# Kernel tuning notes

Measured on AMD Instinct MI355X. Metric: run time of the kernel, lower is better.

Reference implementation:

```python
import jax, jax.numpy as jnp
import numpy as np

B, N, D = 64, 1024, 512
H, LD = 8, 64            # num_heads, linear_hidden_dim (H*LD == D)
HIDDEN = 4 * D           # ffn_multiply = 4.0
NB = 128                 # number of timestamp buckets
EPS = 1e-6
TS_SCALE = NB / 14.0     # log1p(1e6) ~ 13.8 -> buckets span [0, NB]


def rms_norm(x, eps=EPS):
    return x * jax.lax.rsqrt(jnp.mean(x * x, axis=-1, keepdims=True) + eps)


def setup_inputs() -> dict:
    key = jax.random.key(0)
    ks = jax.random.split(key, 8)
    lengths = np.linspace(256, N, B).astype(np.int64)
    x_offsets = jnp.asarray(np.concatenate([[0], np.cumsum(lengths)]), dtype=jnp.int64)
    T = int(lengths.sum())
    x = jax.random.normal(ks[0], (T, D), dtype=jnp.float32)
    all_timestamps = jnp.sort(jax.random.randint(ks[1], (B, N), 0, 10**6, dtype=jnp.int64), axis=1)
    invalid_attn_mask = jnp.tril(jnp.ones((N, N), jnp.float32))  # causal
    uv = jax.random.normal(ks[2], (D, 3 * H * LD), dtype=jnp.float32) * 0.02
    pos_w = jax.random.normal(ks[3], (2 * N - 1,), dtype=jnp.float32) * 0.02
    ts_w = jax.random.normal(ks[4], (NB + 1,), dtype=jnp.float32) * 0.02
    w_ams = jax.random.normal(ks[5], (2 * H * LD, D), dtype=jnp.float32) * 0.02
    w1 = jax.random.normal(ks[6], (D, HIDDEN), dtype=jnp.float32) * 0.02
    w2 = jax.random.normal(ks[7], (HIDDEN, D), dtype=jnp.float32) * 0.02
    return {"x": x, "x_offsets": x_offsets, "all_timestamps": all_timestamps,
            "invalid_attn_mask": invalid_attn_mask, "uv": uv, "pos_w": pos_w,
            "ts_w": ts_w, "w_ams": w_ams, "w1": w1, "w2": w2}


def reference(x, x_offsets, all_timestamps, invalid_attn_mask, uv, pos_w, ts_w, w_ams, w1, w2):
    T = x.shape[0]
    # RMSNorm (no learned scale, matches F.rms_norm with no weight) + fused proj + SiLU
    proj = jax.nn.silu(rms_norm(x) @ uv)                       # [T, 3*H*LD]
    u, v = proj[:, :2 * H * LD], proj[:, 2 * H * LD:]          # [T,2HD'], [T,HD']
    # jagged -> padded dense
    tok = jnp.arange(T)
    seg = jnp.searchsorted(x_offsets, tok, side="right") - 1   # batch id per token
    pos = tok - x_offsets[seg]                                  # position within sequence
    padded_v = jnp.zeros((B, N, H * LD), v.dtype).at[seg, pos].set(v).reshape(B, N, H, LD)
    # positional relative bias (batch-independent)
    rel = jnp.arange(N)[:, None] - jnp.arange(N)[None, :]
    pos_attn = pos_w[rel + N - 1] * invalid_attn_mask           # [N,N]
    # temporal relative bias: log-bucketized |t_i - t_j|
    dt = jnp.abs(all_timestamps[:, :, None] - all_timestamps[:, None, :]).astype(jnp.float32)
    bucket = jnp.clip(jnp.floor(jnp.log1p(dt) * TS_SCALE), 0, NB).astype(jnp.int32)
    ts_attn = ts_w[bucket] * invalid_attn_mask[None]            # [B,N,N]
    # two-stream bias 'attention' (no softmax)
    out_pos = jnp.einsum("nm,bmhd->bnhd", pos_attn, padded_v)
    out_ts = jnp.einsum("bnm,bmhd->bnhd", ts_attn, padded_v)
    combined = jnp.concatenate([out_pos, out_ts], axis=-1).reshape(B, N, 2 * H * LD)
    attn_out = combined[seg, pos]                               # dense -> jagged, [T, 2*H*LD]
    # gated norm + multistage FFN with residuals
    ams = u * rms_norm(attn_out)
    h = x + ams @ w_ams
    out = h + jax.nn.silu(rms_norm(h) @ w1) @ w2
    return out
```

## Files before the change

### kernel.cpp

```cpp
#include <hip/hip_runtime.h>
#include <cmath>


using u16 = unsigned short;
using u8  = unsigned char;

typedef __bf16 bf16x8 __attribute__((ext_vector_type(8)));
typedef float  f32x4  __attribute__((ext_vector_type(4)));

#define TS_SCALE_F (float)(128.0 / 14.0)

__device__ __forceinline__ u16 f2b(float f) {
  unsigned u = __float_as_uint(f);
  unsigned r = 0x7FFFu + ((u >> 16) & 1u);
  return (u16)((u + r) >> 16);
}
__device__ __forceinline__ float b2f(u16 v) {
  return __uint_as_float(((unsigned)v) << 16);
}
__device__ __forceinline__ bf16x8 as_frag(uint4 r) {
  union { uint4 u; bf16x8 v; } c; c.u = r; return c.v;
}

__device__ __forceinline__ void gload_lds16(const u16* g, u16* l) {
  __builtin_amdgcn_global_load_lds(
      (const __attribute__((address_space(1))) unsigned int*)g,
      (__attribute__((address_space(3))) unsigned int*)l, 16, 0, 0);
}

__device__ __forceinline__ size_t ts_base_u8(int b, int nt) {
  return (size_t)b * 589824 + (size_t)(nt * (nt + 1) / 2) * 16384;
}

__global__ __launch_bounds__(256) void wprep(
    const float* __restrict__ W, u16* __restrict__ Wp, int K, int N)
{
  const int p = blockIdx.x, s = blockIdx.y;
  const int t = threadIdx.x;
  size_t base = ((size_t)p * (K >> 5) + s) * 4096;
  const int e0 = t * 16;
  u16 o[16];
#pragma unroll
  for (int i = 0; i < 16; ++i) {
    int e = e0 + i;
    int kb = e >> 10, r = e & 1023, c = r >> 3, ke = r & 7;
    o[i] = f2b(W[(size_t)(s * 32 + kb * 8 + ke) * N + p * 128 + c]);
  }
  *(uint4*)(Wp + base + e0)     = *(uint4*)o;
  *(uint4*)(Wp + base + e0 + 8) = *(uint4*)(o + 8);
}

#define EPI_SILU_BF16 0
#define EPI_ADD_F32   1
#define AM_BF16   0
#define AM_F32S   1
#define AM_BF16SM 2

template <int EPI, int AMODE>
__global__ __launch_bounds__(256, 2) void gemm_bf16(
    const u16* __restrict__ A, const float* __restrict__ Af,
    const float* __restrict__ inv, const u16* __restrict__ U, int ustride,
    const u16* __restrict__ Wp, void* __restrict__ C,
    const float* __restrict__ ADD, int M, int N, int K, int ncb)
{
  __shared__ u16 lA[128 * 40];
  __shared__ u16 lB[4096];

  const int nblk = gridDim.x;
  const int q = nblk >> 3, r = nblk & 7;
  const int xcd = blockIdx.x & 7, li = blockIdx.x >> 3;
  const int work = xcd * q + (xcd < r ? xcd : r) + li;
  const int c0b = work % ncb;
  const int t0  = (work / ncb) * 128;
  const int c0  = c0b * 128;

  const int tid  = threadIdx.x;
  const int wave = tid >> 6, lane = tid & 63;
  const int wr   = (wave >> 1) * 64, wc = (wave & 1) * 64;
  const int l15  = lane & 15, l4 = lane >> 4;

  f32x4 z = {0.f, 0.f, 0.f, 0.f};
  f32x4 acc[4][4];
#pragma unroll
  for (int m = 0; m < 4; ++m)
#pragma unroll
    for (int j = 0; j < 4; ++j) acc[m][j] = z;

  const int ar = tid >> 1, ak = (tid & 1) * 16;
  const int row = t0 + ar;
  const bool arow_ok = row < M;
  float rinv = 0.f;
  if (AMODE != AM_BF16 && arow_ok) rinv = inv[row];
  const u16*   ab = (AMODE != AM_F32S) ? A + (size_t)row * K + ak : nullptr;
  const float* af = (AMODE == AM_F32S) ? Af + (size_t)row * K + ak : nullptr;
  const u16*   um = (AMODE == AM_BF16SM) ? U + (size_t)row * ustride + ak : nullptr;

  const int ksteps = K >> 5;
  const u16* wsrc = Wp + (size_t)c0b * ksteps * 4096 + wave * 1024 + lane * 8;
  u16* ldsb = &lB[wave * 1024];

  for (int s = 0; s < ksteps; ++s) {
    const int k0 = s * 32;
    uint4 pr[4];
    const uint4 z4 = make_uint4(0, 0, 0, 0);
    if (!arow_ok) { pr[0] = z4; pr[1] = z4; pr[2] = z4; pr[3] = z4; }
    else if constexpr (AMODE == AM_BF16) {
      pr[0] = *(const uint4*)(ab + k0);
      pr[1] = *(const uint4*)(ab + k0 + 8);
    } else if constexpr (AMODE == AM_F32S) {
      pr[0] = *(const uint4*)(af + k0);
      pr[1] = *(const uint4*)(af + k0 + 4);
      pr[2] = *(const uint4*)(af + k0 + 8);
      pr[3] = *(const uint4*)(af + k0 + 12);
    } else {
      pr[0] = *(const uint4*)(ab + k0);
      pr[1] = *(const uint4*)(ab + k0 + 8);
      pr[2] = *(const uint4*)(um + k0);
      pr[3] = *(const uint4*)(um + k0 + 8);
    }
    gload_lds16(wsrc,       ldsb);
    gload_lds16(wsrc + 512, ldsb + 512);
    wsrc += 4096;
    {
      u16 tmp[16];
      if constexpr (AMODE == AM_BF16) {
        *(uint4*)tmp       = pr[0];
        *(uint4*)(tmp + 8) = pr[1];
      } else if constexpr (AMODE == AM_F32S) {
        const float* f = (const float*)pr;
#pragma unroll
        for (int i = 0; i < 16; ++i) tmp[i] = f2b(f[i] * rinv);
      } else {
        const u16* a = (const u16*)pr;
        const u16* u = (const u16*)(pr + 2);
#pragma unroll
        for (int i = 0; i < 16; ++i) tmp[i] = f2b(b2f(a[i]) * rinv * b2f(u[i]));
      }
      *(uint4*)&lA[ar * 40 + ak]     = *(uint4*)tmp;
      *(uint4*)&lA[ar * 40 + ak + 8] = *(uint4*)(tmp + 8);
    }
    __syncthreads();

    bf16x8 afr[4], bfv[4];
#pragma unroll
    for (int m = 0; m < 4; ++m)
      afr[m] = as_frag(*(const uint4*)&lA[(wr + m * 16 + l15) * 40 + l4 * 8]);
#pragma unroll
    for (int j = 0; j < 4; ++j)
      bfv[j] = as_frag(*(const uint4*)&lB[(l4 << 10) + (wc + j * 16 + l15) * 8]);
#pragma unroll
    for (int m = 0; m < 4; ++m)
#pragma unroll
      for (int j = 0; j < 4; ++j)
        acc[m][j] = __builtin_amdgcn_mfma_f32_16x16x32_bf16(afr[m], bfv[j], acc[m][j], 0, 0, 0);
    __syncthreads();
  }

#pragma unroll
  for (int m = 0; m < 4; ++m) {
#pragma unroll
    for (int rr = 0; rr < 4; ++rr) {
      int orow = t0 + wr + m * 16 + l4 * 4 + rr;
      if (orow >= M) continue;
#pragma unroll
      for (int j = 0; j < 4; ++j) {
        int col = c0 + wc + j * 16 + l15;
        size_t idx = (size_t)orow * N + col;
        float y = acc[m][j][rr];
        if constexpr (EPI == EPI_SILU_BF16) {
          float s = y / (1.f + __expf(-y));
          ((u16*)C)[idx] = f2b(s);
        } else {
          ((float*)C)[idx] = y + ADD[idx];
        }
      }
    }
  }
}

__global__ __launch_bounds__(128) void pos_scores(
    const float* __restrict__ pos_w, u16* __restrict__ pos_s)
{
  const int n = blockIdx.x;
  const int m0 = threadIdx.x * 8;
  u16 o[8];
#pragma unroll
  for (int i = 0; i < 8; ++i) {
    int m = m0 + i;
    float v = (m <= n) ? pos_w[n - m + 1023] : 0.f;
    o[i] = f2b(v);
  }
  *(uint4*)(pos_s + (size_t)n * 1024 + m0) = *(uint4*)o;
}

__global__ __launch_bounds__(256) void ts_buckets(
    const int* __restrict__ tstamp, u8* __restrict__ ts_s)
{
  const int nt = 7 - (blockIdx.x >> 6);
  const int b  = blockIdx.x & 63;
  const int W  = 128 * (nt + 1);
  const int n0 = nt * 128;
  const int tid = threadIdx.x;

  __shared__ int tsm[1024];
  for (int i = tid; i < W; i += 256) tsm[i] = tstamp[b * 1024 + i];
  __syncthreads();

  const int r = tid >> 1, h = tid & 1;
  const int n_abs = n0 + r;
  const int t_n = tstamp[b * 1024 + n_abs];
  const int half = W >> 1;
  const int c0 = h * half;
  u8* row = ts_s + ts_base_u8(b, nt) + (size_t)r * W + c0;

  for (int c = 0; c < half; c += 16) {
    u8 o[16];
#pragma unroll
    for (int i = 0; i < 16; ++i) {
      int m = c0 + c + i;
      int d = t_n - tsm[m];
      if (d < 0) d = -d;
      int bkt = (int)(log1pf((float)d) * TS_SCALE_F);
      bkt = bkt > 128 ? 128 : bkt;
      o[i] = (m <= n_abs) ? (u8)bkt : (u8)129;
    }
    *(uint4*)(row + c) = *(uint4*)o;
  }
}

__global__ __launch_bounds__(256, 1) void attn_gemm(
    const u16* __restrict__ proj,
    const int* __restrict__ xoff,
    const u16* __restrict__ pos_s,
    const u8*  __restrict__ tsU8,
    const float* __restrict__ ts_w,
    u16* __restrict__ attn_out,
    int Ttot)
{
  const int flat = blockIdx.x;
  const int nt = 7 - (flat >> 8);
  const int rem = flat & 255;
  const int b  = rem >> 2;
  const int ct = rem & 3;

  const int off = xoff[b];
  int len = xoff[b + 1] - off;
  if (len < 0) len = 0;
  if (len > 1024) len = 1024;
  if (off < 0 || off + len > Ttot) return;
  const int n0 = nt * 128;
  if (n0 >= len) return;
  const int c0 = ct * 128;
  const int W = 128 * (nt + 1);

  __shared__ u16 lP[128 * 40];
  __shared__ u16 lT[128 * 40];
  __shared__ u16 sV[4096];
  __shared__ float s_tsw[130];

  const int tid = threadIdx.x;
  if (tid < 130) s_tsw[tid] = (tid < 129) ? ts_w[tid] : 0.f;
  __syncthreads();

  const int wave = tid >> 6, lane = tid & 63;
  const int wr = (wave >> 1) * 64, wc = (wave & 1) * 64;
  const int l15 = lane & 15, l4 = lane >> 4;

  f32x4 z = {0.f, 0.f, 0.f, 0.f};
  f32x4 accP[4][4], accT[4][4];
#pragma unroll
  for (int m = 0; m < 4; ++m)
#pragma unroll
    for (int j = 0; j < 4; ++j) { accP[m][j] = z; accT[m][j] = z; }

  const int ar = tid >> 1, ak = (tid & 1) * 16;
  const u16* pRow = pos_s + (size_t)(n0 + ar) * 1024 + ak;
  const u8*  tRow = tsU8 + ts_base_u8(b, nt) + (size_t)ar * W + ak;
  const int vk = tid >> 3, vc = (tid & 7) * 16;

  const int mEnd = (n0 + 128 < len) ? (n0 + 128) : len;

  for (int m0 = 0; m0 < mEnd; m0 += 32) {
    {
      int mm = m0 + vk;
      uint4 v0 = make_uint4(0, 0, 0, 0), v1 = v0;
      if (mm < len) {
        const u16* src = proj + (size_t)(off + mm) * 1536 + 1024 + c0 + vc;
        v0 = *(const uint4*)src;
        v1 = *(const uint4*)(src + 8);
      }
      u16 tmp[16];
      *(uint4*)tmp       = v0;
      *(uint4*)(tmp + 8) = v1;
      const int kb = vk >> 3, ke = vk & 7;
#pragma unroll
      for (int i = 0; i < 16; ++i) {
        int col = vc + i;
        int o2 = (kb * 2048 + col * 16 + ke * 2) ^ (((col >> 3) & 7) << 4);
        *(u16*)((char*)sV + o2) = tmp[i];
      }
    }
    {
      uint4 p0 = *(const uint4*)(pRow + m0);
      uint4 p1 = *(const uint4*)(pRow + m0 + 8);
      uint4 tb = *(const uint4*)(tRow + m0);
      u16 tt[16];
      const u8* bp = (const u8*)&tb;
#pragma unroll
      for (int i = 0; i < 16; ++i) tt[i] = f2b(s_tsw[bp[i]]);
      int wb = ar * 40 + ak;
      *(uint4*)&lP[wb]     = p0;
      *(uint4*)&lP[wb + 8] = p1;
      *(uint4*)&lT[wb]     = *(uint4*)tt;
      *(uint4*)&lT[wb + 8] = *(uint4*)(tt + 8);
    }
    __syncthreads();

    bf16x8 ap[4], at[4], bv[4];
#pragma unroll
    for (int m = 0; m < 4; ++m) {
      ap[m] = as_frag(*(const uint4*)&lP[(wr + m * 16 + l15) * 40 + l4 * 8]);
      at[m] = as_frag(*(const uint4*)&lT[(wr + m * 16 + l15) * 40 + l4 * 8]);
    }
#pragma unroll
    for (int j = 0; j < 4; ++j) {
      int col = wc + j * 16 + l15;
      int o2 = (l4 * 2048 + col * 16) ^ (((col >> 3) & 7) << 4);
      bv[j] = as_frag(*(const uint4*)((char*)sV + o2));
    }
#pragma unroll
    for (int m = 0; m < 4; ++m)
#pragma unroll
      for (int j = 0; j < 4; ++j) {
        accP[m][j] = __builtin_amdgcn_mfma_f32_16x16x32_bf16(ap[m], bv[j], accP[m][j], 0, 0, 0);
        accT[m][j] = __builtin_amdgcn_mfma_f32_16x16x32_bf16(at[m], bv[j], accT[m][j], 0, 0, 0);
      }
    __syncthreads();
  }

#pragma unroll
  for (int m = 0; m < 4; ++m)
#pragma unroll
    for (int r = 0; r < 4; ++r) {
      int n = n0 + wr + m * 16 + l4 * 4 + r;
      if (n >= len) continue;
      size_t t = (size_t)(off + n);
#pragma unroll
      for (int j = 0; j < 4; ++j) {
        int hd = c0 + wc + j * 16 + l15;
        int colP = ((hd >> 6) << 7) + (hd & 63);
        attn_out[t * 1024 + colP]      = f2b(accP[m][j][r]);
        attn_out[t * 1024 + colP + 64] = f2b(accT[m][j][r]);
      }
    }
}

template <int D, bool F32IN>
__global__ __launch_bounds__(256) void row_ss(
    const void* __restrict__ in, float* __restrict__ inv, int T)
{
  const int row = blockIdx.x * 4 + (threadIdx.x >> 6);
  const int lane = threadIdx.x & 63;
  if (row >= T) return;
  float ss = 0.f;
  if constexpr (F32IN) {
    const float* r = (const float*)in + (size_t)row * D;
#pragma unroll
    for (int i = lane * 4; i < D; i += 256) {
      float4 v = *(const float4*)(r + i);
      ss += v.x * v.x + v.y * v.y + v.z * v.z + v.w * v.w;
    }
  } else {
    const u16* r = (const u16*)in + (size_t)row * D;
#pragma unroll
    for (int i = lane * 8; i < D; i += 512) {
      uint4 v = *(const uint4*)(r + i);
      const u16* q = (const u16*)&v;
#pragma unroll
      for (int k = 0; k < 8; ++k) { float f = b2f(q[k]); ss += f * f; }
    }
  }
#pragma unroll
  for (int o = 32; o > 0; o >>= 1) ss += __shfl_down(ss, o, 64);
  if (lane == 0) inv[row] = rsqrtf(ss / (float)D + 1e-6f);
}

extern "C" void kernel_launch(void* const* d_in, const int* in_sizes, int n_in,
                              void* d_out, int out_size, void* d_ws, size_t ws_size,
                              hipStream_t stream)
{
  const float* x      = (const float*)d_in[0];
  const int*   xoff   = (const int*)d_in[1];
  const int*   tstamp = (const int*)d_in[2];
  const float* uv     = (const float*)d_in[4];
  const float* pos_w  = (const float*)d_in[5];
  const float* ts_w   = (const float*)d_in[6];
  const float* w_ams  = (const float*)d_in[7];
  const float* w1     = (const float*)d_in[8];
  const float* w2     = (const float*)d_in[9];
  const int T = in_sizes[0] / 512;
  const int nrow = (T + 127) / 128;

  char* ws = (char*)d_ws;
  size_t o = 0;
  auto take = [&](size_t bytes) { size_t r = o; o += (bytes + 255) & ~(size_t)255; return r; };

  u16* uvb    = (u16*)(ws + take((size_t)512 * 1536 * 2));
  u16* wamsb  = (u16*)(ws + take((size_t)1024 * 512 * 2));
  u16* w1b    = (u16*)(ws + take((size_t)512 * 2048 * 2));
  u16* w2b    = (u16*)(ws + take((size_t)2048 * 512 * 2));
  u16* posS   = (u16*)(ws + take((size_t)1024 * 1024 * 2));

  size_t o_ts   = take((size_t)64 * 589824);
  size_t o_attn = take((size_t)T * 1024 * 2);
  size_t o_proj = take((size_t)T * 1536 * 2);
  float* invX = (float*)(ws + take((size_t)T * 4));
  float* invA = (float*)(ws + take((size_t)T * 4));
  float* invH = (float*)(ws + take((size_t)T * 4));

  u8*  tsU8  = (u8*)(ws + o_ts);
  u16* attnS = (u16*)(ws + o_attn);
  u16* proj  = (u16*)(ws + o_proj);
  u16* mid   = (u16*)(ws + o_ts);
  float* h   = (float*)d_out;

  if (ws_size < o) return;

  wprep<<<dim3(12, 16), 256, 0, stream>>>(uv,    uvb,   512,  1536);
  wprep<<<dim3(4, 32),  256, 0, stream>>>(w_ams, wamsb, 1024, 512);
  wprep<<<dim3(16, 16), 256, 0, stream>>>(w1,    w1b,   512,  2048);
  wprep<<<dim3(4, 64),  256, 0, stream>>>(w2,    w2b,   2048, 512);

  pos_scores<<<1024, 128, 0, stream>>>(pos_w, posS);
  ts_buckets<<<512, 256, 0, stream>>>(tstamp, tsU8);

  row_ss<512, true><<<(T + 3) / 4, 256, 0, stream>>>(x, invX, T);

  gemm_bf16<EPI_SILU_BF16, AM_F32S><<<12 * nrow, 256, 0, stream>>>(
      nullptr, x, invX, nullptr, 0, uvb, proj, nullptr, T, 1536, 512, 12);

  attn_gemm<<<64 * 32, 256, 0, stream>>>(proj, xoff, posS, tsU8, ts_w, attnS, T);

  row_ss<1024, false><<<(T + 3) / 4, 256, 0, stream>>>(attnS, invA, T);

  gemm_bf16<EPI_ADD_F32, AM_BF16SM><<<4 * nrow, 256, 0, stream>>>(
      attnS, nullptr, invA, proj, 1536, wamsb, h, x, T, 512, 1024, 4);

  row_ss<512, true><<<(T + 3) / 4, 256, 0, stream>>>(h, invH, T);

  gemm_bf16<EPI_SILU_BF16, AM_F32S><<<16 * nrow, 256, 0, stream>>>(
      nullptr, h, invH, nullptr, 0, w1b, mid, nullptr, T, 2048, 512, 16);

  gemm_bf16<EPI_ADD_F32, AM_BF16><<<4 * nrow, 256, 0, stream>>>(
      mid, nullptr, nullptr, nullptr, 0, w2b, h, h, T, 512, 2048, 4);
}
```

Measured before the change: 855.2 us.

## Pre-pack V into MFMA layout and stream it via direct-to-LDS loads

Adds a vprep kernel that repacks the V slice of proj into the MFMA B-fragment tile layout, staged in the output buffer. attn_gemm can then fetch V with global_load_lds instead of scalar swizzled LDS stores. It also remaps block indices so consecutive blocks spread across XCDs, and switches bf16 rounding to the hardware packed convert. The costs are an extra kernel launch with a strided repack pass, and the output buffer now serves as scratch space.

New measurement: 877.8 us. 1.03x slower.

```diff
diff --git a/kernel.cpp b/kernel.cpp
--- a/kernel.cpp
+++ b/kernel.cpp
@@ -6,7 +6,9 @@
 using u8  = unsigned char;
 
 typedef __bf16 bf16x8 __attribute__((ext_vector_type(8)));
+typedef __bf16 bf16x2 __attribute__((ext_vector_type(2)));
 typedef float  f32x4  __attribute__((ext_vector_type(4)));
+typedef float  f32x2  __attribute__((ext_vector_type(2)));
 
 #define TS_SCALE_F (float)(128.0 / 14.0)
 
@@ -14,6 +16,14 @@
   unsigned u = __float_as_uint(f);
   unsigned r = 0x7FFFu + ((u >> 16) & 1u);
   return (u16)((u + r) >> 16);
+}
+__device__ __forceinline__ u16 f2b_n(float f) {
+  union { __bf16 b; u16 u; } c; c.b = (__bf16)f; return c.u;
+}
+__device__ __forceinline__ unsigned cvt_pk2(float a, float b) {
+  f32x2 v; v[0] = a; v[1] = b;
+  bf16x2 r = __builtin_convertvector(v, bf16x2);
+  union { bf16x2 b; unsigned u; } c; c.b = r; return c.u;
 }
 __device__ __forceinline__ float b2f(u16 v) {
   return __uint_as_float(((unsigned)v) << 16);
@@ -48,6 +58,38 @@
   }
   *(uint4*)(Wp + base + e0)     = *(uint4*)o;
   *(uint4*)(Wp + base + e0 + 8) = *(uint4*)(o + 8);
+}
+
+__global__ __launch_bounds__(256) void vprep(
+    const u16* __restrict__ proj, const int* __restrict__ xoff,
+    u16* __restrict__ Vp, int Ttot)
+{
+  const int b = blockIdx.x >> 5, rb = blockIdx.x & 31;
+  const int off = xoff[b];
+  int len = xoff[b + 1] - off;
+  if (len < 0) len = 0;
+  if (len > 1024) len = 1024;
+  if (off < 0 || off + len > Ttot) return;
+  if (rb * 32 >= len) return;
+  const int t = threadIdx.x;
+  size_t base = ((size_t)(b * 32 + rb)) * 4 * 4096;
+  const int e0 = t * 16;
+#pragma unroll
+  for (int ct = 0; ct < 4; ++ct) {
+    u16 o[16];
+#pragma unroll
+    for (int i = 0; i < 16; ++i) {
+      int e = e0 + i;
+      int kb = e >> 10, r = e & 1023, c = r >> 3, ke = r & 7;
+      int row = rb * 32 + kb * 8 + ke;
+      u16 v = 0;
+      if (row < len)
+        v = proj[(size_t)(off + row) * 1536 + 1024 + ct * 128 + c];
+      o[i] = v;
+    }
+    *(uint4*)(Vp + base + ct * 4096 + e0)     = *(uint4*)o;
+    *(uint4*)(Vp + base + ct * 4096 + e0 + 8) = *(uint4*)(o + 8);
+  }
 }
 
 #define EPI_SILU_BF16 0
@@ -123,18 +165,22 @@
     wsrc += 4096;
     {
       u16 tmp[16];
+      unsigned* t32 = (unsigned*)tmp;
       if constexpr (AMODE == AM_BF16) {
         *(uint4*)tmp       = pr[0];
         *(uint4*)(tmp + 8) = pr[1];
       } else if constexpr (AMODE == AM_F32S) {
         const float* f = (const float*)pr;
 #pragma unroll
-        for (int i = 0; i < 16; ++i) tmp[i] = f2b(f[i] * rinv);
+        for (int i = 0; i < 8; ++i)
+          t32[i] = cvt_pk2(f[2 * i] * rinv, f[2 * i + 1] * rinv);
       } else {
         const u16* a = (const u16*)pr;
         const u16* u = (const u16*)(pr + 2);
 #pragma unroll
-        for (int i = 0; i < 16; ++i) tmp[i] = f2b(b2f(a[i]) * rinv * b2f(u[i]));
+        for (int i = 0; i < 8; ++i)
+          t32[i] = cvt_pk2(b2f(a[2 * i]) * rinv * b2f(u[2 * i]),
+                           b2f(a[2 * i + 1]) * rinv * b2f(u[2 * i + 1]));
       }
       *(uint4*)&lA[ar * 40 + ak]     = *(uint4*)tmp;
       *(uint4*)&lA[ar * 40 + ak + 8] = *(uint4*)(tmp + 8);
@@ -169,7 +215,7 @@
         float y = acc[m][j][rr];
         if constexpr (EPI == EPI_SILU_BF16) {
           float s = y / (1.f + __expf(-y));
-          ((u16*)C)[idx] = f2b(s);
+          ((u16*)C)[idx] = f2b_n(s);
         } else {
           ((float*)C)[idx] = y + ADD[idx];
         }
@@ -229,7 +275,7 @@
 }
 
 __global__ __launch_bounds__(256, 1) void attn_gemm(
-    const u16* __restrict__ proj,
+    const u16* __restrict__ Vp,
     const int* __restrict__ xoff,
     const u16* __restrict__ pos_s,
     const u8*  __restrict__ tsU8,
@@ -237,11 +283,11 @@
     u16* __restrict__ attn_out,
     int Ttot)
 {
-  const int flat = blockIdx.x;
-  const int nt = 7 - (flat >> 8);
-  const int rem = flat & 255;
-  const int b  = rem >> 2;
-  const int ct = rem & 3;
+  const int li = blockIdx.x >> 3, xcd = blockIdx.x & 7;
+  const int sblk = xcd + (li >> 2) * 8;
+  const int ct = li & 3;
+  const int nt = 7 - (sblk >> 6);
+  const int b  = sblk & 63;
 
   const int off = xoff[b];
   int len = xoff[b + 1] - off;
@@ -276,43 +322,29 @@
   const int ar = tid >> 1, ak = (tid & 1) * 16;
   const u16* pRow = pos_s + (size_t)(n0 + ar) * 1024 + ak;
   const u8*  tRow = tsU8 + ts_base_u8(b, nt) + (size_t)ar * W + ak;
-  const int vk = tid >> 3, vc = (tid & 7) * 16;
+  const u16* vbase = Vp + ((size_t)(b * 32) * 4 + ct) * 4096 + wave * 1024 + lane * 8;
+  u16* ldsv = &sV[wave * 1024];
 
   const int mEnd = (n0 + 128 < len) ? (n0 + 128) : len;
 
   for (int m0 = 0; m0 < mEnd; m0 += 32) {
-    {
-      int mm = m0 + vk;
-      uint4 v0 = make_uint4(0, 0, 0, 0), v1 = v0;
-      if (mm < len) {
-        const u16* src = proj + (size_t)(off + mm) * 1536 + 1024 + c0 + vc;
-        v0 = *(const uint4*)src;
-        v1 = *(const uint4*)(src + 8);
-      }
-      u16 tmp[16];
-      *(uint4*)tmp       = v0;
-      *(uint4*)(tmp + 8) = v1;
-      const int kb = vk >> 3, ke = vk & 7;
-#pragma unroll
-      for (int i = 0; i < 16; ++i) {
-        int col = vc + i;
-        int o2 = (kb * 2048 + col * 16 + ke * 2) ^ (((col >> 3) & 7) << 4);
-        *(u16*)((char*)sV + o2) = tmp[i];
-      }
-    }
+    const u16* vsrc = vbase + (size_t)(m0 >> 5) * 16384;
+    gload_lds16(vsrc,       ldsv);
+    gload_lds16(vsrc + 512, ldsv + 512);
     {
       uint4 p0 = *(const uint4*)(pRow + m0);
       uint4 p1 = *(const uint4*)(pRow + m0 + 8);
       uint4 tb = *(const uint4*)(tRow + m0);
-      u16 tt[16];
       const u8* bp = (const u8*)&tb;
-#pragma unroll
-      for (int i = 0; i < 16; ++i) tt[i] = f2b(s_tsw[bp[i]]);
+      unsigned tt32[8];
+#pragma unroll
+      for (int i = 0; i < 8; ++i)
+        tt32[i] = cvt_pk2(s_tsw[bp[2 * i]], s_tsw[bp[2 * i + 1]]);
       int wb = ar * 40 + ak;
       *(uint4*)&lP[wb]     = p0;
       *(uint4*)&lP[wb + 8] = p1;
-      *(uint4*)&lT[wb]     = *(uint4*)tt;
-      *(uint4*)&lT[wb + 8] = *(uint4*)(tt + 8);
+      *(uint4*)&lT[wb]     = *(uint4*)tt32;
+      *(uint4*)&lT[wb + 8] = *(uint4*)(tt32 + 4);
     }
     __syncthreads();
 
@@ -323,11 +355,8 @@
       at[m] = as_frag(*(const uint4*)&lT[(wr + m * 16 + l15) * 40 + l4 * 8]);
     }
 #pragma unroll
-    for (int j = 0; j < 4; ++j) {
-      int col = wc + j * 16 + l15;
-      int o2 = (l4 * 2048 + col * 16) ^ (((col >> 3) & 7) << 4);
-      bv[j] = as_frag(*(const uint4*)((char*)sV + o2));
-    }
+    for (int j = 0; j < 4; ++j)
+      bv[j] = as_frag(*(const uint4*)&sV[(l4 << 10) + (wc + j * 16 + l15) * 8]);
 #pragma unroll
     for (int m = 0; m < 4; ++m)
 #pragma unroll
@@ -349,8 +378,8 @@
       for (int j = 0; j < 4; ++j) {
         int hd = c0 + wc + j * 16 + l15;
         int colP = ((hd >> 6) << 7) + (hd & 63);
-        attn_out[t * 1024 + colP]      = f2b(accP[m][j][r]);
-        attn_out[t * 1024 + colP + 64] = f2b(accT[m][j][r]);
+        attn_out[t * 1024 + colP]      = f2b_n(accP[m][j][r]);
+        attn_out[t * 1024 + colP + 64] = f2b_n(accT[m][j][r]);
       }
     }
 }
@@ -411,7 +440,7 @@
   u16* w2b    = (u16*)(ws + take((size_t)2048 * 512 * 2));
   u16* posS   = (u16*)(ws + take((size_t)1024 * 1024 * 2));
 
-  size_t o_ts   = take((size_t)64 * 589824);
+  size_t o_ts   = take((size_t)64 * 589824 + 256);
   size_t o_attn = take((size_t)T * 1024 * 2);
   size_t o_proj = take((size_t)T * 1536 * 2);
   float* invX = (float*)(ws + take((size_t)T * 4));
@@ -422,6 +451,7 @@
   u16* attnS = (u16*)(ws + o_attn);
   u16* proj  = (u16*)(ws + o_proj);
   u16* mid   = (u16*)(ws + o_ts);
+  u16*   Vp  = (u16*)d_out;
   float* h   = (float*)d_out;
 
   if (ws_size < o) return;
@@ -439,7 +469,9 @@
   gemm_bf16<EPI_SILU_BF16, AM_F32S><<<12 * nrow, 256, 0, stream>>>(
       nullptr, x, invX, nullptr, 0, uvb, proj, nullptr, T, 1536, 512, 12);
 
-  attn_gemm<<<64 * 32, 256, 0, stream>>>(proj, xoff, posS, tsU8, ts_w, attnS, T);
+  vprep<<<2048, 256, 0, stream>>>(proj, xoff, Vp, T);
+
+  attn_gemm<<<64 * 32, 256, 0, stream>>>(Vp, xoff, posS, tsU8, ts_w, attnS, T);
 
   row_ss<1024, false><<<(T + 3) / 4, 256, 0, stream>>>(attnS, invA, T);
 
```

## Double GEMM K-step to 64 and use native packed bf16 conversion

Applied to the files above, without the earlier changes.

Each GEMM main-loop iteration now stages a K-depth of 64 instead of 32, enlarging the A and B LDS tiles and running two MFMA sub-steps per barrier pair. This halves the number of __syncthreads and loop iterations per tile, at the cost of more LDS and registers per block, which may hurt occupancy at 2 blocks/CU. Manual round-to-nearest-even bf16 conversions are also replaced with compiler vector conversions (packed cvt) in the GEMM prologue, the epilogues and the attention T-matrix build. The workspace ts region gets 256 bytes of padding.

New measurement: 906.4 us. 6.0% more time.

```diff
diff --git a/kernel.cpp b/kernel.cpp
--- a/kernel.cpp
+++ b/kernel.cpp
@@ -6,7 +6,9 @@
 using u8  = unsigned char;
 
 typedef __bf16 bf16x8 __attribute__((ext_vector_type(8)));
+typedef __bf16 bf16x2 __attribute__((ext_vector_type(2)));
 typedef float  f32x4  __attribute__((ext_vector_type(4)));
+typedef float  f32x2  __attribute__((ext_vector_type(2)));
 
 #define TS_SCALE_F (float)(128.0 / 14.0)
 
@@ -14,6 +16,14 @@
   unsigned u = __float_as_uint(f);
   unsigned r = 0x7FFFu + ((u >> 16) & 1u);
   return (u16)((u + r) >> 16);
+}
+__device__ __forceinline__ u16 f2b_n(float f) {
+  union { __bf16 b; u16 u; } c; c.b = (__bf16)f; return c.u;
+}
+__device__ __forceinline__ unsigned cvt_pk2(float a, float b) {
+  f32x2 v; v[0] = a; v[1] = b;
+  bf16x2 r = __builtin_convertvector(v, bf16x2);
+  union { bf16x2 b; unsigned u; } c; c.b = r; return c.u;
 }
 __device__ __forceinline__ float b2f(u16 v) {
   return __uint_as_float(((unsigned)v) << 16);
@@ -63,8 +73,8 @@
     const u16* __restrict__ Wp, void* __restrict__ C,
     const float* __restrict__ ADD, int M, int N, int K, int ncb)
 {
-  __shared__ u16 lA[128 * 40];
-  __shared__ u16 lB[4096];
+  __shared__ u16 lA[128 * 72];
+  __shared__ u16 lB[8192];
 
   const int nblk = gridDim.x;
   const int q = nblk >> 3, r = nblk & 7;
@@ -86,7 +96,7 @@
 #pragma unroll
     for (int j = 0; j < 4; ++j) acc[m][j] = z;
 
-  const int ar = tid >> 1, ak = (tid & 1) * 16;
+  const int ar = tid >> 1, ak = (tid & 1) * 32;
   const int row = t0 + ar;
   const bool arow_ok = row < M;
   float rinv = 0.f;
@@ -95,64 +105,74 @@
   const float* af = (AMODE == AM_F32S) ? Af + (size_t)row * K + ak : nullptr;
   const u16*   um = (AMODE == AM_BF16SM) ? U + (size_t)row * ustride + ak : nullptr;
 
-  const int ksteps = K >> 5;
-  const u16* wsrc = Wp + (size_t)c0b * ksteps * 4096 + wave * 1024 + lane * 8;
-  u16* ldsb = &lB[wave * 1024];
-
-  for (int s = 0; s < ksteps; ++s) {
-    const int k0 = s * 32;
-    uint4 pr[4];
+  const int rounds = K >> 6;
+  const u16* wsrc = Wp + (size_t)c0b * (K >> 5) * 4096 + wave * 2048 + lane * 8;
+  u16* ldsb = &lB[wave * 2048];
+
+  for (int s = 0; s < rounds; ++s) {
+    const int k0 = s * 64;
+    uint4 pr[8];
     const uint4 z4 = make_uint4(0, 0, 0, 0);
-    if (!arow_ok) { pr[0] = z4; pr[1] = z4; pr[2] = z4; pr[3] = z4; }
-    else if constexpr (AMODE == AM_BF16) {
-      pr[0] = *(const uint4*)(ab + k0);
-      pr[1] = *(const uint4*)(ab + k0 + 8);
+    if (!arow_ok) {
+#pragma unroll
+      for (int i = 0; i < 8; ++i) pr[i] = z4;
+    } else if constexpr (AMODE == AM_BF16) {
+#pragma unroll
+      for (int i = 0; i < 4; ++i) pr[i] = *(const uint4*)(ab + k0 + 8 * i);
     } else if constexpr (AMODE == AM_F32S) {
-      pr[0] = *(const uint4*)(af + k0);
-      pr[1] = *(const uint4*)(af + k0 + 4);
-      pr[2] = *(const uint4*)(af + k0 + 8);
-      pr[3] = *(const uint4*)(af + k0 + 12);
+#pragma unroll
+      for (int i = 0; i < 8; ++i) pr[i] = *(const uint4*)(af + k0 + 4 * i);
     } else {
-      pr[0] = *(const uint4*)(ab + k0);
-      pr[1] = *(const uint4*)(ab + k0 + 8);
-      pr[2] = *(const uint4*)(um + k0);
-      pr[3] = *(const uint4*)(um + k0 + 8);
-    }
-    gload_lds16(wsrc,       ldsb);
-    gload_lds16(wsrc + 512, ldsb + 512);
-    wsrc += 4096;
+#pragma unroll
+      for (int i = 0; i < 4; ++i) pr[i] = *(const uint4*)(ab + k0 + 8 * i);
+#pragma unroll
+      for (int i = 0; i < 4; ++i) pr[4 + i] = *(const uint4*)(um + k0 + 8 * i);
+    }
+    gload_lds16(wsrc,        ldsb);
+    gload_lds16(wsrc + 512,  ldsb + 512);
+    gload_lds16(wsrc + 1024, ldsb + 1024);
+    gload_lds16(wsrc + 1536, ldsb + 1536);
+    wsrc += 8192;
     {
-      u16 tmp[16];
+      u16 tmp[32];
+      unsigned* t32 = (unsigned*)tmp;
       if constexpr (AMODE == AM_BF16) {
-        *(uint4*)tmp       = pr[0];
-        *(uint4*)(tmp + 8) = pr[1];
+#pragma unroll
+        for (int i = 0; i < 4; ++i) *(uint4*)(tmp + 8 * i) = pr[i];
       } else if constexpr (AMODE == AM_F32S) {
         const float* f = (const float*)pr;
 #pragma unroll
-        for (int i = 0; i < 16; ++i) tmp[i] = f2b(f[i] * rinv);
+        for (int i = 0; i < 16; ++i)
+          t32[i] = cvt_pk2(f[2 * i] * rinv, f[2 * i + 1] * rinv);
       } else {
         const u16* a = (const u16*)pr;
-        const u16* u = (const u16*)(pr + 2);
-#pragma unroll
-        for (int i = 0; i < 16; ++i) tmp[i] = f2b(b2f(a[i]) * rinv * b2f(u[i]));
-      }
-      *(uint4*)&lA[ar * 40 + ak]     = *(uint4*)tmp;
-      *(uint4*)&lA[ar * 40 + ak + 8] = *(uint4*)(tmp + 8);
+        const u16* u = (const u16*)(pr + 4);
+#pragma unroll
+        for (int i = 0; i < 16; ++i)
+          t32[i] = cvt_pk2(b2f(a[2 * i]) * rinv * b2f(u[2 * i]),
+                           b2f(a[2 * i + 1]) * rinv * b2f(u[2 * i + 1]));
+      }
+#pragma unroll
+      for (int i = 0; i < 4; ++i)
+        *(uint4*)&lA[ar * 72 + ak + 8 * i] = *(uint4*)(tmp + 8 * i);
     }
     __syncthreads();
 
-    bf16x8 afr[4], bfv[4];
-#pragma unroll
-    for (int m = 0; m < 4; ++m)
-      afr[m] = as_frag(*(const uint4*)&lA[(wr + m * 16 + l15) * 40 + l4 * 8]);
-#pragma unroll
-    for (int j = 0; j < 4; ++j)
-      bfv[j] = as_frag(*(const uint4*)&lB[(l4 << 10) + (wc + j * 16 + l15) * 8]);
-#pragma unroll
-    for (int m = 0; m < 4; ++m)
+#pragma unroll
+    for (int ks = 0; ks < 2; ++ks) {
+      bf16x8 afr[4], bfv[4];
+#pragma unroll
+      for (int m = 0; m < 4; ++m)
+        afr[m] = as_frag(*(const uint4*)&lA[(wr + m * 16 + l15) * 72 + ks * 32 + l4 * 8]);
 #pragma unroll
       for (int j = 0; j < 4; ++j)
-        acc[m][j] = __builtin_amdgcn_mfma_f32_16x16x32_bf16(afr[m], bfv[j], acc[m][j], 0, 0, 0);
+        bfv[j] = as_frag(*(const uint4*)&lB[ks * 4096 + (l4 << 10) + (wc + j * 16 + l15) * 8]);
+#pragma unroll
+      for (int m = 0; m < 4; ++m)
+#pragma unroll
+        for (int j = 0; j < 4; ++j)
+          acc[m][j] = __builtin_amdgcn_mfma_f32_16x16x32_bf16(afr[m], bfv[j], acc[m][j], 0, 0, 0);
+    }
     __syncthreads();
   }
 
@@ -169,7 +189,7 @@
         float y = acc[m][j][rr];
         if constexpr (EPI == EPI_SILU_BF16) {
           float s = y / (1.f + __expf(-y));
-          ((u16*)C)[idx] = f2b(s);
+          ((u16*)C)[idx] = f2b_n(s);
         } else {
           ((float*)C)[idx] = y + ADD[idx];
         }
@@ -304,15 +324,16 @@
       uint4 p0 = *(const uint4*)(pRow + m0);
       uint4 p1 = *(const uint4*)(pRow + m0 + 8);
       uint4 tb = *(const uint4*)(tRow + m0);
-      u16 tt[16];
       const u8* bp = (const u8*)&tb;
-#pragma unroll
-      for (int i = 0; i < 16; ++i) tt[i] = f2b(s_tsw[bp[i]]);
+      unsigned tt32[8];
+#pragma unroll
+      for (int i = 0; i < 8; ++i)
+        tt32[i] = cvt_pk2(s_tsw[bp[2 * i]], s_tsw[bp[2 * i + 1]]);
       int wb = ar * 40 + ak;
       *(uint4*)&lP[wb]     = p0;
       *(uint4*)&lP[wb + 8] = p1;
-      *(uint4*)&lT[wb]     = *(uint4*)tt;
-      *(uint4*)&lT[wb + 8] = *(uint4*)(tt + 8);
+      *(uint4*)&lT[wb]     = *(uint4*)tt32;
+      *(uint4*)&lT[wb + 8] = *(uint4*)(tt32 + 4);
     }
     __syncthreads();
 
@@ -349,8 +370,8 @@
       for (int j = 0; j < 4; ++j) {
         int hd = c0 + wc + j * 16 + l15;
         int colP = ((hd >> 6) << 7) + (hd & 63);
-        attn_out[t * 1024 + colP]      = f2b(accP[m][j][r]);
-        attn_out[t * 1024 + colP + 64] = f2b(accT[m][j][r]);
+        attn_out[t * 1024 + colP]      = f2b_n(accP[m][j][r]);
+        attn_out[t * 1024 + colP + 64] = f2b_n(accT[m][j][r]);
       }
     }
 }
@@ -411,7 +432,7 @@
   u16* w2b    = (u16*)(ws + take((size_t)2048 * 512 * 2));
   u16* posS   = (u16*)(ws + take((size_t)1024 * 1024 * 2));
 
-  size_t o_ts   = take((size_t)64 * 589824);
+  size_t o_ts   = take((size_t)64 * 589824 + 256);
   size_t o_attn = take((size_t)T * 1024 * 2);
   size_t o_proj = take((size_t)T * 1536 * 2);
   float* invX = (float*)(ws + take((size_t)T * 4));
```

## Pre-tile GEMM A operands into LDS image layout and use packed bf16 conversion

Applied to the files above, without the earlier changes.

The RMS-norm pass for x now also writes a normalized bf16 copy of x in a tiled image layout, parked in the output buffer. The FFN1 GEMM epilogue writes its SiLU output in the same tiled layout. The uv and w2 GEMMs then load their A tiles straight into LDS with global_load_lds instead of per-thread register loads, conversion and LDS stores. Manual bf16 rounding is also replaced by the hardware packed float-to-bf16 conversion in several places. The cost is a scattered 2-byte epilogue store pattern for the image writes, and the tiled x image relies on the output buffer being free until the w_ams GEMM writes h.

Result: faster. 834.0 us (-2.5%).

```diff
diff --git a/kernel.cpp b/kernel.cpp
--- a/kernel.cpp
+++ b/kernel.cpp
@@ -6,7 +6,9 @@
 using u8  = unsigned char;
 
 typedef __bf16 bf16x8 __attribute__((ext_vector_type(8)));
+typedef __bf16 bf16x2 __attribute__((ext_vector_type(2)));
 typedef float  f32x4  __attribute__((ext_vector_type(4)));
+typedef float  f32x2  __attribute__((ext_vector_type(2)));
 
 #define TS_SCALE_F (float)(128.0 / 14.0)
 
@@ -14,6 +16,14 @@
   unsigned u = __float_as_uint(f);
   unsigned r = 0x7FFFu + ((u >> 16) & 1u);
   return (u16)((u + r) >> 16);
+}
+__device__ __forceinline__ u16 f2b_n(float f) {
+  union { __bf16 b; u16 u; } c; c.b = (__bf16)f; return c.u;
+}
+__device__ __forceinline__ unsigned cvt_pk2(float a, float b) {
+  f32x2 v; v[0] = a; v[1] = b;
+  bf16x2 r = __builtin_convertvector(v, bf16x2);
+  union { bf16x2 b; unsigned u; } c; c.b = r; return c.u;
 }
 __device__ __forceinline__ float b2f(u16 v) {
   return __uint_as_float(((unsigned)v) << 16);
@@ -52,9 +62,11 @@
 
 #define EPI_SILU_BF16 0
 #define EPI_ADD_F32   1
+#define EPI_SILU_IMG  2
 #define AM_BF16   0
 #define AM_F32S   1
 #define AM_BF16SM 2
+#define AM_IMG    3
 
 template <int EPI, int AMODE>
 __global__ __launch_bounds__(256, 2) void gemm_bf16(
@@ -90,51 +102,64 @@
   const int row = t0 + ar;
   const bool arow_ok = row < M;
   float rinv = 0.f;
-  if (AMODE != AM_BF16 && arow_ok) rinv = inv[row];
-  const u16*   ab = (AMODE != AM_F32S) ? A + (size_t)row * K + ak : nullptr;
+  if (AMODE == AM_F32S || AMODE == AM_BF16SM) if (arow_ok) rinv = inv[row];
+  const u16*   ab = (AMODE == AM_BF16 || AMODE == AM_BF16SM)
+                        ? A + (size_t)row * K + ak : nullptr;
   const float* af = (AMODE == AM_F32S) ? Af + (size_t)row * K + ak : nullptr;
   const u16*   um = (AMODE == AM_BF16SM) ? U + (size_t)row * ustride + ak : nullptr;
 
   const int ksteps = K >> 5;
   const u16* wsrc = Wp + (size_t)c0b * ksteps * 4096 + wave * 1024 + lane * 8;
   u16* ldsb = &lB[wave * 1024];
+  const u16* asrc = (AMODE == AM_IMG)
+      ? A + (size_t)(t0 >> 7) * ksteps * 4096 + wave * 1024 + lane * 8
+      : nullptr;
+  u16* ldsa = &lA[wave * 1024];
 
   for (int s = 0; s < ksteps; ++s) {
-    const int k0 = s * 32;
-    uint4 pr[4];
-    const uint4 z4 = make_uint4(0, 0, 0, 0);
-    if (!arow_ok) { pr[0] = z4; pr[1] = z4; pr[2] = z4; pr[3] = z4; }
-    else if constexpr (AMODE == AM_BF16) {
-      pr[0] = *(const uint4*)(ab + k0);
-      pr[1] = *(const uint4*)(ab + k0 + 8);
-    } else if constexpr (AMODE == AM_F32S) {
-      pr[0] = *(const uint4*)(af + k0);
-      pr[1] = *(const uint4*)(af + k0 + 4);
-      pr[2] = *(const uint4*)(af + k0 + 8);
-      pr[3] = *(const uint4*)(af + k0 + 12);
-    } else {
-      pr[0] = *(const uint4*)(ab + k0);
-      pr[1] = *(const uint4*)(ab + k0 + 8);
-      pr[2] = *(const uint4*)(um + k0);
-      pr[3] = *(const uint4*)(um + k0 + 8);
-    }
     gload_lds16(wsrc,       ldsb);
     gload_lds16(wsrc + 512, ldsb + 512);
     wsrc += 4096;
-    {
+    if constexpr (AMODE == AM_IMG) {
+      gload_lds16(asrc,       ldsa);
+      gload_lds16(asrc + 512, ldsa + 512);
+      asrc += 4096;
+    } else {
+      const int k0 = s * 32;
+      uint4 pr[4];
+      const uint4 z4 = make_uint4(0, 0, 0, 0);
+      if (!arow_ok) { pr[0] = z4; pr[1] = z4; pr[2] = z4; pr[3] = z4; }
+      else if constexpr (AMODE == AM_BF16) {
+        pr[0] = *(const uint4*)(ab + k0);
+        pr[1] = *(const uint4*)(ab + k0 + 8);
+      } else if constexpr (AMODE == AM_F32S) {
+        pr[0] = *(const uint4*)(af + k0);
+        pr[1] = *(const uint4*)(af + k0 + 4);
+        pr[2] = *(const uint4*)(af + k0 + 8);
+        pr[3] = *(const uint4*)(af + k0 + 12);
+      } else {
+        pr[0] = *(const uint4*)(ab + k0);
+        pr[1] = *(const uint4*)(ab + k0 + 8);
+        pr[2] = *(const uint4*)(um + k0);
+        pr[3] = *(const uint4*)(um + k0 + 8);
+      }
       u16 tmp[16];
+      unsigned* t32 = (unsigned*)tmp;
       if constexpr (AMODE == AM_BF16) {
         *(uint4*)tmp       = pr[0];
         *(uint4*)(tmp + 8) = pr[1];
       } else if constexpr (AMODE == AM_F32S) {
         const float* f = (const float*)pr;
 #pragma unroll
-        for (int i = 0; i < 16; ++i) tmp[i] = f2b(f[i] * rinv);
-      } else {
+        for (int i = 0; i < 8; ++i)
+          t32[i] = cvt_pk2(f[2 * i] * rinv, f[2 * i + 1] * rinv);
+      } else if constexpr (AMODE == AM_BF16SM) {
         const u16* a = (const u16*)pr;
         const u16* u = (const u16*)(pr + 2);
 #pragma unroll
-        for (int i = 0; i < 16; ++i) tmp[i] = f2b(b2f(a[i]) * rinv * b2f(u[i]));
+        for (int i = 0; i < 8; ++i)
+          t32[i] = cvt_pk2(b2f(a[2 * i]) * rinv * b2f(u[2 * i]),
+                           b2f(a[2 * i + 1]) * rinv * b2f(u[2 * i + 1]));
       }
       *(uint4*)&lA[ar * 40 + ak]     = *(uint4*)tmp;
       *(uint4*)&lA[ar * 40 + ak + 8] = *(uint4*)(tmp + 8);
@@ -143,8 +168,12 @@
 
     bf16x8 afr[4], bfv[4];
 #pragma unroll
-    for (int m = 0; m < 4; ++m)
-      afr[m] = as_frag(*(const uint4*)&lA[(wr + m * 16 + l15) * 40 + l4 * 8]);
+    for (int m = 0; m < 4; ++m) {
+      if constexpr (AMODE == AM_IMG)
+        afr[m] = as_frag(*(const uint4*)&lA[(l4 << 10) + (wr + m * 16 + l15) * 8]);
+      else
+        afr[m] = as_frag(*(const uint4*)&lA[(wr + m * 16 + l15) * 40 + l4 * 8]);
+    }
 #pragma unroll
     for (int j = 0; j < 4; ++j)
       bfv[j] = as_frag(*(const uint4*)&lB[(l4 << 10) + (wc + j * 16 + l15) * 8]);
@@ -165,13 +194,19 @@
 #pragma unroll
       for (int j = 0; j < 4; ++j) {
         int col = c0 + wc + j * 16 + l15;
-        size_t idx = (size_t)orow * N + col;
         float y = acc[m][j][rr];
         if constexpr (EPI == EPI_SILU_BF16) {
           float s = y / (1.f + __expf(-y));
-          ((u16*)C)[idx] = f2b(s);
+          ((u16*)C)[(size_t)orow * N + col] = f2b_n(s);
+        } else if constexpr (EPI == EPI_ADD_F32) {
+          size_t idx = (size_t)orow * N + col;
+          ((float*)C)[idx] = y + ADD[idx];
         } else {
-          ((float*)C)[idx] = y + ADD[idx];
+          float s = y / (1.f + __expf(-y));
+          size_t ioff = ((size_t)(t0 >> 7) * (N >> 5) + (col >> 5)) * 4096
+                      + (size_t)((col >> 3) & 3) * 1024
+                      + (size_t)(orow & 127) * 8 + (col & 7);
+          ((u16*)C)[ioff] = f2b_n(s);
         }
       }
     }
@@ -304,15 +339,16 @@
       uint4 p0 = *(const uint4*)(pRow + m0);
       uint4 p1 = *(const uint4*)(pRow + m0 + 8);
       uint4 tb = *(const uint4*)(tRow + m0);
-      u16 tt[16];
       const u8* bp = (const u8*)&tb;
-#pragma unroll
-      for (int i = 0; i < 16; ++i) tt[i] = f2b(s_tsw[bp[i]]);
+      unsigned tt32[8];
+#pragma unroll
+      for (int i = 0; i < 8; ++i)
+        tt32[i] = cvt_pk2(s_tsw[bp[2 * i]], s_tsw[bp[2 * i + 1]]);
       int wb = ar * 40 + ak;
       *(uint4*)&lP[wb]     = p0;
       *(uint4*)&lP[wb + 8] = p1;
-      *(uint4*)&lT[wb]     = *(uint4*)tt;
-      *(uint4*)&lT[wb + 8] = *(uint4*)(tt + 8);
+      *(uint4*)&lT[wb]     = *(uint4*)tt32;
+      *(uint4*)&lT[wb + 8] = *(uint4*)(tt32 + 4);
     }
     __syncthreads();
 
@@ -349,26 +385,37 @@
       for (int j = 0; j < 4; ++j) {
         int hd = c0 + wc + j * 16 + l15;
         int colP = ((hd >> 6) << 7) + (hd & 63);
-        attn_out[t * 1024 + colP]      = f2b(accP[m][j][r]);
-        attn_out[t * 1024 + colP + 64] = f2b(accT[m][j][r]);
-      }
-    }
-}
-
-template <int D, bool F32IN>
+        attn_out[t * 1024 + colP]      = f2b_n(accP[m][j][r]);
+        attn_out[t * 1024 + colP + 64] = f2b_n(accT[m][j][r]);
+      }
+    }
+}
+
+template <int D, bool F32IN, bool WIMG>
 __global__ __launch_bounds__(256) void row_ss(
-    const void* __restrict__ in, float* __restrict__ inv, int T)
+    const void* __restrict__ in, float* __restrict__ inv, u16* __restrict__ img,
+    int T)
 {
   const int row = blockIdx.x * 4 + (threadIdx.x >> 6);
   const int lane = threadIdx.x & 63;
   if (row >= T) return;
   float ss = 0.f;
+  float v8[8];
   if constexpr (F32IN) {
     const float* r = (const float*)in + (size_t)row * D;
-#pragma unroll
-    for (int i = lane * 4; i < D; i += 256) {
-      float4 v = *(const float4*)(r + i);
-      ss += v.x * v.x + v.y * v.y + v.z * v.z + v.w * v.w;
+    if constexpr (WIMG) {
+      float4 a = *(const float4*)(r + lane * 8);
+      float4 b = *(const float4*)(r + lane * 8 + 4);
+      v8[0] = a.x; v8[1] = a.y; v8[2] = a.z; v8[3] = a.w;
+      v8[4] = b.x; v8[5] = b.y; v8[6] = b.z; v8[7] = b.w;
+#pragma unroll
+      for (int k = 0; k < 8; ++k) ss += v8[k] * v8[k];
+    } else {
+#pragma unroll
+      for (int i = lane * 4; i < D; i += 256) {
+        float4 v = *(const float4*)(r + i);
+        ss += v.x * v.x + v.y * v.y + v.z * v.z + v.w * v.w;
+      }
     }
   } else {
     const u16* r = (const u16*)in + (size_t)row * D;
@@ -382,7 +429,19 @@
   }
 #pragma unroll
   for (int o = 32; o > 0; o >>= 1) ss += __shfl_down(ss, o, 64);
-  if (lane == 0) inv[row] = rsqrtf(ss / (float)D + 1e-6f);
+  ss = __shfl(ss, 0, 64);
+  float rv = rsqrtf(ss / (float)D + 1e-6f);
+  if (lane == 0) inv[row] = rv;
+  if constexpr (WIMG) {
+    unsigned w[4];
+#pragma unroll
+    for (int i = 0; i < 4; ++i)
+      w[i] = cvt_pk2(v8[2 * i] * rv, v8[2 * i + 1] * rv);
+    size_t off = (size_t)(row >> 7) * ((D >> 5) * 4096)
+               + (size_t)(lane >> 2) * 4096 + (size_t)(lane & 3) * 1024
+               + (size_t)(row & 127) * 8;
+    *(uint4*)(img + off) = *(uint4*)w;
+  }
 }
 
 extern "C" void kernel_launch(void* const* d_in, const int* in_sizes, int n_in,
@@ -411,7 +470,7 @@
   u16* w2b    = (u16*)(ws + take((size_t)2048 * 512 * 2));
   u16* posS   = (u16*)(ws + take((size_t)1024 * 1024 * 2));
 
-  size_t o_ts   = take((size_t)64 * 589824);
+  size_t o_ts   = take((size_t)64 * 589824 + 256);
   size_t o_attn = take((size_t)T * 1024 * 2);
   size_t o_proj = take((size_t)T * 1536 * 2);
   float* invX = (float*)(ws + take((size_t)T * 4));
@@ -421,7 +480,8 @@
   u8*  tsU8  = (u8*)(ws + o_ts);
   u16* attnS = (u16*)(ws + o_attn);
   u16* proj  = (u16*)(ws + o_proj);
-  u16* mid   = (u16*)(ws + o_ts);
+  u16* midI  = (u16*)(ws + o_ts);
+  u16*   xb  = (u16*)d_out;
   float* h   = (float*)d_out;
 
   if (ws_size < o) return;
@@ -434,23 +494,23 @@
   pos_scores<<<1024, 128, 0, stream>>>(pos_w, posS);
   ts_buckets<<<512, 256, 0, stream>>>(tstamp, tsU8);
 
-  row_ss<512, true><<<(T + 3) / 4, 256, 0, stream>>>(x, invX, T);
-
-  gemm_bf16<EPI_SILU_BF16, AM_F32S><<<12 * nrow, 256, 0, stream>>>(
-      nullptr, x, invX, nullptr, 0, uvb, proj, nullptr, T, 1536, 512, 12);
+  row_ss<512, true, true><<<(T + 3) / 4, 256, 0, stream>>>(x, invX, xb, T);
+
+  gemm_bf16<EPI_SILU_BF16, AM_IMG><<<12 * nrow, 256, 0, stream>>>(
+      xb, nullptr, nullptr, nullptr, 0, uvb, proj, nullptr, T, 1536, 512, 12);
 
   attn_gemm<<<64 * 32, 256, 0, stream>>>(proj, xoff, posS, tsU8, ts_w, attnS, T);
 
-  row_ss<1024, false><<<(T + 3) / 4, 256, 0, stream>>>(attnS, invA, T);
+  row_ss<1024, false, false><<<(T + 3) / 4, 256, 0, stream>>>(attnS, invA, nullptr, T);
 
   gemm_bf16<EPI_ADD_F32, AM_BF16SM><<<4 * nrow, 256, 0, stream>>>(
       attnS, nullptr, invA, proj, 1536, wamsb, h, x, T, 512, 1024, 4);
 
-  row_ss<512, true><<<(T + 3) / 4, 256, 0, stream>>>(h, invH, T);
-
-  gemm_bf16<EPI_SILU_BF16, AM_F32S><<<16 * nrow, 256, 0, stream>>>(
-      nullptr, h, invH, nullptr, 0, w1b, mid, nullptr, T, 2048, 512, 16);
-
-  gemm_bf16<EPI_ADD_F32, AM_BF16><<<4 * nrow, 256, 0, stream>>>(
-      mid, nullptr, nullptr, nullptr, 0, w2b, h, h, T, 512, 2048, 4);
-}
+  row_ss<512, true, false><<<(T + 3) / 4, 256, 0, stream>>>(h, invH, nullptr, T);
+
+  gemm_bf16<EPI_SILU_IMG, AM_F32S><<<16 * nrow, 256, 0, stream>>>(
+      nullptr, h, invH, nullptr, 0, w1b, midI, nullptr, T, 2048, 512, 16);
+
+  gemm_bf16<EPI_ADD_F32, AM_IMG><<<4 * nrow, 256, 0, stream>>>(
+      midI, nullptr, nullptr, nullptr, 0, w2b, h, h, T, 512, 2048, 4);
+}
```
